# Kernel tuning notes

Hardware: AMD Instinct MI355X
Metric: run time of the kernel (lower is better)

## Reference

```python
import jax, jax.numpy as jnp
import numpy as np

NUM_HEADS = 16
HEAD_DIM = 64
HIDDEN = NUM_HEADS * HEAD_DIM
LN_EPS = 1e-6


def setup_inputs() -> dict:
    key = jax.random.key(0)
    ks = jax.random.split(key, 5)
    B, T, H = 2, 2048, HIDDEN
    s = 1.0 / np.sqrt(H)
    return {
        "h": jax.random.normal(ks[0], (B, T, H), jnp.float32),
        "Wq": jax.random.normal(ks[1], (H, H), jnp.float32) * s,
        "bq": jnp.zeros((H,), jnp.float32),
        "Wk": jax.random.normal(ks[2], (H, H), jnp.float32) * s,
        "bk": jnp.zeros((H,), jnp.float32),
        "Wv": jax.random.normal(ks[3], (H, H), jnp.float32) * s,
        "bv": jnp.zeros((H,), jnp.float32),
        "Wo": jax.random.normal(ks[4], (H, H), jnp.float32) * s,
        "bo": jnp.zeros((H,), jnp.float32),
        "gamma": jnp.ones((H,), jnp.float32),
        "beta": jnp.zeros((H,), jnp.float32),
    }


def _split_heads(x):
    B, T, H = x.shape
    return x.reshape(B, T, NUM_HEADS, HEAD_DIM).transpose(0, 2, 1, 3)  # [B,h,T,d]


def reference(h, Wq, bq, Wk, bk, Wv, bv, Wo, bo, gamma, beta):
    # QKV projections (nn.Linear: x @ W^T + b)
    Q = _split_heads(h @ Wq.T + bq)
    K = _split_heads(h @ Wk.T + bk)
    V = _split_heads(h @ Wv.T + bv)
    scale = HEAD_DIM ** -0.5
    scores = jnp.einsum("bhqd,bhkd->bhqk", Q, K) * scale  # [B,h,T,T]
    attn = jax.nn.softmax(scores, axis=-1)
    ctx = jnp.einsum("bhqk,bhkd->bhqd", attn, V)          # [B,h,T,d]
    B, _, T, _ = ctx.shape
    ctx = ctx.transpose(0, 2, 1, 3).reshape(B, T, HIDDEN)
    out = ctx @ Wo.T + bo + h  # dropout is identity at eval
    # LayerNorm(eps=1e-6)
    mu = out.mean(-1, keepdims=True)
    var = jnp.mean((out - mu) ** 2, -1, keepdims=True)
    return (out - mu) * jax.lax.rsqrt(var + LN_EPS) * gamma + beta
```

## Files before the change

### kernel.cpp

```cpp
#include <hip/hip_runtime.h>
#include <hip/hip_bf16.h>

#define NH   16
#define HD   64
#define HID  1024
#define TSEQ 2048
#define BATCH 2
#define KSCALE 0.18033688011112042f

typedef __attribute__((ext_vector_type(4))) float f32x4;
typedef __attribute__((ext_vector_type(8))) short s16x8;
typedef __attribute__((ext_vector_type(4))) short s16x4;
typedef __attribute__((ext_vector_type(8))) _Float16 f16x8;
typedef __attribute__((ext_vector_type(4))) _Float16 f16x4;
typedef __attribute__((ext_vector_type(2))) _Float16 f16x2;

__device__ __forceinline__ unsigned short f2bf(float f) {
  union { float f; unsigned int u; } v; v.f = f;
  unsigned int r = v.u + 0x7fffu + ((v.u >> 16) & 1u);
  return (unsigned short)(r >> 16);
}
__device__ __forceinline__ float bf2f(unsigned short b) {
  union { unsigned int u; float f; } v; v.u = ((unsigned int)b) << 16; return v.f;
}

__device__ __forceinline__ void gll16(const void* g, void* l) {
  __builtin_amdgcn_global_load_lds(
      (const __attribute__((address_space(1))) unsigned int*)g,
      (__attribute__((address_space(3))) unsigned int*)l, 16, 0, 0);
}

__global__ __launch_bounds__(256) void cast_all_k(
    const float* __restrict__ h,
    const float* __restrict__ w0, const float* __restrict__ w1,
    const float* __restrict__ w2, const float* __restrict__ w3,
    unsigned short* __restrict__ hb, unsigned short* __restrict__ wbase) {
  int i = blockIdx.x * 256 + threadIdx.x;
  const float* src; unsigned short* dst; int idx; float sc = 1.f;
  if (i < 1048576) { src = h; dst = hb; idx = i; }
  else {
    int idx4 = i - 1048576;
    int w = idx4 >> 18;
    idx = idx4 & 262143;
    src = (w == 0) ? w0 : (w == 1) ? w1 : (w == 2) ? w2 : w3;
    dst = wbase + (size_t)(idx4 - idx) * 4;
    if (w == 1) sc = KSCALE;
  }
  float4 v = ((const float4*)src)[idx];
  ushort4 o;
  o.x = f2bf(v.x * sc); o.y = f2bf(v.y * sc); o.z = f2bf(v.z * sc); o.w = f2bf(v.w * sc);
  ((ushort4*)dst)[idx] = o;
}

__global__ __launch_bounds__(256) void gemm_qkv(
    const unsigned short* __restrict__ hb,
    const unsigned short* __restrict__ wcat,
    const float* __restrict__ bq, const float* __restrict__ bk, const float* __restrict__ bv,
    unsigned short* __restrict__ qo, unsigned short* __restrict__ ko,
    unsigned short* __restrict__ vto) {
  __shared__ unsigned short Ash[2][128 * 32];
  __shared__ unsigned short Bsh[2][128 * 32];
  const int tid = threadIdx.x, lane = tid & 63, wave = tid >> 6;
  const int l15 = lane & 15, quad = lane >> 4;
  const int wr = wave >> 1, wc = wave & 1;
  const int bn = blockIdx.x * 128, bm = blockIdx.y * 128;
  const char* Ab = (const char*)(hb + (size_t)bm * HID);
  const char* Bb = (const char*)(wcat + (size_t)bn * HID);
  const int off = tid * 16;
  const int r0 = off >> 6, c0 = off & 63;
  const size_t ga0 = (size_t)r0 * (HID * 2) + c0;
  const size_t ga1 = (size_t)(r0 + 64) * (HID * 2) + c0;
  const int lb0 = wave * 512;
  const int lb1 = 2048 + wave * 512;

  f32x4 acc[4][4];
#pragma unroll
  for (int i = 0; i < 4; ++i)
#pragma unroll
    for (int j = 0; j < 4; ++j) acc[i][j] = f32x4{0.f, 0.f, 0.f, 0.f};

  gll16(Ab + ga0, &Ash[0][lb0]);
  gll16(Ab + ga1, &Ash[0][lb1]);
  gll16(Bb + ga0, &Bsh[0][lb0]);
  gll16(Bb + ga1, &Bsh[0][lb1]);
  __syncthreads();

  for (int k0 = 0; k0 < HID; k0 += 32) {
    const int cur = (k0 >> 5) & 1;
    if (k0 + 32 < HID) {
      const size_t kb = (size_t)(k0 + 32) * 2;
      gll16(Ab + ga0 + kb, &Ash[cur ^ 1][lb0]);
      gll16(Ab + ga1 + kb, &Ash[cur ^ 1][lb1]);
      gll16(Bb + ga0 + kb, &Bsh[cur ^ 1][lb0]);
      gll16(Bb + ga1 + kb, &Bsh[cur ^ 1][lb1]);
    }
    s16x8 af[4], bfr[4];
#pragma unroll
    for (int i = 0; i < 4; ++i)
      af[i] = *(const s16x8*)(&Ash[cur][(wr * 64 + i * 16 + l15) * 32 + quad * 8]);
#pragma unroll
    for (int j = 0; j < 4; ++j)
      bfr[j] = *(const s16x8*)(&Bsh[cur][(wc * 64 + j * 16 + l15) * 32 + quad * 8]);
#pragma unroll
    for (int i = 0; i < 4; ++i)
#pragma unroll
      for (int j = 0; j < 4; ++j)
        acc[i][j] = __builtin_amdgcn_mfma_f32_16x16x32_bf16(af[i], bfr[j], acc[i][j], 0, 0, 0);
    __syncthreads();
  }

  const int mat = bn >> 10;
  const int cb = (bn & 1023) + wc * 64;
  const int rbase = bm + wr * 64;
  if (mat == 2) {
#pragma unroll
    for (int j = 0; j < 4; ++j) {
      const int coln = cb + j * 16 + l15;
      const int head = coln >> 6, d = coln & 63;
      const float bb = bv[coln];
#pragma unroll
      for (int i = 0; i < 4; ++i) {
        const int row0 = rbase + i * 16 + quad * 4;
        const int bI = row0 >> 11, t0 = row0 & 2047;
        unsigned short o[4];
#pragma unroll
        for (int r = 0; r < 4; ++r) {
          _Float16 hv = (_Float16)(acc[i][j][r] + bb);
          o[r] = __builtin_bit_cast(unsigned short, hv);
        }
        *(s16x4*)(vto + ((size_t)((bI * NH + head) * HD + d)) * TSEQ + t0) = *(const s16x4*)o;
      }
    }
  } else {
    unsigned short* dst = (mat == 0) ? qo : ko;
#pragma unroll
    for (int j = 0; j < 4; ++j) {
      const int coln = cb + j * 16 + l15;
      const int head = coln >> 6, d = coln & 63;
      const float bb = (mat == 0) ? bq[coln] : bk[coln] * KSCALE;
#pragma unroll
      for (int i = 0; i < 4; ++i) {
#pragma unroll
        for (int r = 0; r < 4; ++r) {
          const int row = rbase + i * 16 + quad * 4 + r;
          const int bI = row >> 11, t = row & 2047;
          dst[(((size_t)(bI * NH + head) * TSEQ) + t) * HD + d] = f2bf(acc[i][j][r] + bb);
        }
      }
    }
  }
}

__global__ __launch_bounds__(256) void gemm_out(
    const unsigned short* __restrict__ ctx, const unsigned short* __restrict__ wo,
    const float* __restrict__ bo, const float* __restrict__ hres,
    float* __restrict__ outf) {
  __shared__ unsigned short Ash[2][128 * 32];
  __shared__ unsigned short Bsh[2][64 * 32];
  const int tid = threadIdx.x, lane = tid & 63, wave = tid >> 6;
  const int l15 = lane & 15, quad = lane >> 4;
  const int wr = wave >> 1, wc = wave & 1;
  const int bn = blockIdx.x * 64, bm = blockIdx.y * 128;
  const char* Ab = (const char*)(ctx + (size_t)bm * HID);
  const char* Bb = (const char*)(wo + (size_t)bn * HID);
  const int off = tid * 16;
  const int r0 = off >> 6, c0 = off & 63;
  const size_t ga0 = (size_t)r0 * (HID * 2) + c0;
  const size_t ga1 = (size_t)(r0 + 64) * (HID * 2) + c0;
  const int lb0 = wave * 512, lb1 = 2048 + wave * 512;

  f32x4 acc[4][2];
#pragma unroll
  for (int i = 0; i < 4; ++i)
#pragma unroll
    for (int j = 0; j < 2; ++j) acc[i][j] = f32x4{0.f, 0.f, 0.f, 0.f};

  gll16(Ab + ga0, &Ash[0][lb0]);
  gll16(Ab + ga1, &Ash[0][lb1]);
  gll16(Bb + ga0, &Bsh[0][lb0]);
  __syncthreads();

  for (int k0 = 0; k0 < HID; k0 += 32) {
    const int cur = (k0 >> 5) & 1;
    if (k0 + 32 < HID) {
      const size_t kb = (size_t)(k0 + 32) * 2;
      gll16(Ab + ga0 + kb, &Ash[cur ^ 1][lb0]);
      gll16(Ab + ga1 + kb, &Ash[cur ^ 1][lb1]);
      gll16(Bb + ga0 + kb, &Bsh[cur ^ 1][lb0]);
    }
    s16x8 af[4], bfr[2];
#pragma unroll
    for (int i = 0; i < 4; ++i)
      af[i] = *(const s16x8*)(&Ash[cur][(wr * 64 + i * 16 + l15) * 32 + quad * 8]);
#pragma unroll
    for (int j = 0; j < 2; ++j)
      bfr[j] = *(const s16x8*)(&Bsh[cur][(wc * 32 + j * 16 + l15) * 32 + quad * 8]);
#pragma unroll
    for (int i = 0; i < 4; ++i)
#pragma unroll
      for (int j = 0; j < 2; ++j)
        acc[i][j] = __builtin_amdgcn_mfma_f32_16x16x32_bf16(af[i], bfr[j], acc[i][j], 0, 0, 0);
    __syncthreads();
  }
#pragma unroll
  for (int j = 0; j < 2; ++j) {
    const int col = bn + wc * 32 + j * 16 + l15;
    const float bb = bo[col];
#pragma unroll
    for (int i = 0; i < 4; ++i) {
#pragma unroll
      for (int r = 0; r < 4; ++r) {
        const int row = bm + wr * 64 + i * 16 + quad * 4 + r;
        const size_t o = (size_t)row * HID + col;
        outf[o] = acc[i][j][r] + bb + hres[o];
      }
    }
  }
}

__global__ __launch_bounds__(256, 2) void attn_k(
    const unsigned short* __restrict__ qb, const unsigned short* __restrict__ kb,
    const unsigned short* __restrict__ vt, unsigned short* __restrict__ ctx,
    unsigned short* __restrict__ Opart, float* __restrict__ rsumP,
    int lsplit, int ntiles) {
  __shared__ unsigned short Ksh[64 * 72];
  __shared__ unsigned short Vsh[64 * 72];

  const int tid = threadIdx.x, lane = tid & 63, wave = tid >> 6;
  const int l15 = lane & 15, quad = lane >> 4;
  const int z = blockIdx.z;
  const int b = z >> lsplit;
  const int part = z & ((1 << lsplit) - 1);
  const int h = blockIdx.y, qt = blockIdx.x;
  const size_t ho = ((size_t)(b * NH + h)) * TSEQ * HD;
  const unsigned short* Qh = qb + ho;
  const unsigned short* Kh = kb + ho;
  const unsigned short* Vh = vt + ho;
  const int q0 = qt * 128 + wave * 32;
  const int kt0 = part * ntiles;

  s16x8 qf[2][2];
#pragma unroll
  for (int s = 0; s < 2; ++s)
#pragma unroll
    for (int ks = 0; ks < 2; ++ks)
      qf[s][ks] = *(const s16x8*)(Qh + (size_t)(q0 + s * 16 + l15) * HD + ks * 32 + quad * 8);

  f32x4 accO[4][2];
  float rsum[2];
#pragma unroll
  for (int n2 = 0; n2 < 4; ++n2)
#pragma unroll
    for (int s = 0; s < 2; ++s) accO[n2][s] = f32x4{0.f, 0.f, 0.f, 0.f};
  rsum[0] = rsum[1] = 0.f;

  const int sr = tid >> 3, sc = (tid & 7) * 8;
  s16x8 kreg[2], vreg[2];
#pragma unroll
  for (int hf = 0; hf < 2; ++hf) {
    kreg[hf] = *(const s16x8*)(Kh + (size_t)(kt0 * 64 + sr + hf * 32) * HD + sc);
    vreg[hf] = *(const s16x8*)(Vh + (size_t)(sr + hf * 32) * TSEQ + kt0 * 64 + sc);
  }

  for (int kt = 0; kt < ntiles; ++kt) {
    __syncthreads();
#pragma unroll
    for (int hf = 0; hf < 2; ++hf) {
      *(s16x8*)(Ksh + (sr + hf * 32) * 72 + sc) = kreg[hf];
      *(s16x8*)(Vsh + (sr + hf * 32) * 72 + sc) = vreg[hf];
    }
    __syncthreads();
    if (kt + 1 < ntiles) {
      const int k0n = (kt0 + kt + 1) * 64;
#pragma unroll
      for (int hf = 0; hf < 2; ++hf) {
        kreg[hf] = *(const s16x8*)(Kh + (size_t)(k0n + sr + hf * 32) * HD + sc);
        vreg[hf] = *(const s16x8*)(Vh + (size_t)(sr + hf * 32) * TSEQ + k0n + sc);
      }
    }

    f32x4 accS[2][4];
#pragma unroll
    for (int s = 0; s < 2; ++s)
#pragma unroll
      for (int n = 0; n < 4; ++n) accS[s][n] = f32x4{0.f, 0.f, 0.f, 0.f};
#pragma unroll
    for (int ks = 0; ks < 2; ++ks) {
#pragma unroll
      for (int n = 0; n < 4; ++n) {
        s16x8 kf = *(const s16x8*)(Ksh + (n * 16 + l15) * 72 + ks * 32 + quad * 8);
#pragma unroll
        for (int s = 0; s < 2; ++s)
          accS[s][n] = __builtin_amdgcn_mfma_f32_16x16x32_bf16(kf, qf[s][ks], accS[s][n], 0, 0, 0);
      }
    }

    f16x4 pB[2][4];
#pragma unroll
    for (int s = 0; s < 2; ++s)
#pragma unroll
      for (int n = 0; n < 4; ++n) {
        float e0 = __builtin_amdgcn_exp2f(accS[s][n][0]);
        float e1 = __builtin_amdgcn_exp2f(accS[s][n][1]);
        float e2 = __builtin_amdgcn_exp2f(accS[s][n][2]);
        float e3 = __builtin_amdgcn_exp2f(accS[s][n][3]);
        rsum[s] += (e0 + e1) + (e2 + e3);
        f16x2 lo = __builtin_bit_cast(f16x2, __builtin_amdgcn_cvt_pkrtz(e0, e1));
        f16x2 hi = __builtin_bit_cast(f16x2, __builtin_amdgcn_cvt_pkrtz(e2, e3));
        pB[s][n] = f16x4{lo[0], lo[1], hi[0], hi[1]};
      }

#pragma unroll
    for (int n = 0; n < 4; ++n) {
#pragma unroll
      for (int n2 = 0; n2 < 4; ++n2) {
        f16x4 vA = *(const f16x4*)(Vsh + (n2 * 16 + l15) * 72 + n * 16 + quad * 4);
#pragma unroll
        for (int s = 0; s < 2; ++s)
          accO[n2][s] = __builtin_amdgcn_mfma_f32_16x16x16f16(vA, pB[s][n], accO[n2][s], 0, 0, 0);
      }
    }
  }

#pragma unroll
  for (int s = 0; s < 2; ++s) {
    float t = rsum[s];
    t += __shfl_xor(t, 16, 64);
    t += __shfl_xor(t, 32, 64);
    rsum[s] = t;
  }

  if (lsplit) {
    const int slot = (part * BATCH + b) * NH + h;
    const size_t ob = (size_t)slot * TSEQ * HD;
#pragma unroll
    for (int s = 0; s < 2; ++s) {
      const int t = q0 + s * 16 + l15;
#pragma unroll
      for (int n2 = 0; n2 < 4; ++n2) {
        const int d0 = n2 * 16 + quad * 4;
        unsigned short o[4];
#pragma unroll
        for (int r = 0; r < 4; ++r) o[r] = f2bf(accO[n2][s][r]);
        *(s16x4*)(Opart + ob + (size_t)t * HD + d0) = *(const s16x4*)o;
      }
    }
    if (quad == 0) {
      const size_t rb = (size_t)slot * TSEQ;
#pragma unroll
      for (int s = 0; s < 2; ++s)
        rsumP[rb + q0 + s * 16 + l15] = rsum[s];
    }
  } else {
#pragma unroll
    for (int s = 0; s < 2; ++s) {
      const int t = q0 + s * 16 + l15;
      const float inv = 1.f / rsum[s];
#pragma unroll
      for (int n2 = 0; n2 < 4; ++n2) {
        const int d0 = n2 * 16 + quad * 4;
        unsigned short o[4];
#pragma unroll
        for (int r = 0; r < 4; ++r) o[r] = f2bf(accO[n2][s][r] * inv);
        *(s16x4*)(ctx + ((size_t)(b * TSEQ + t)) * HID + h * HD + d0) = *(const s16x4*)o;
      }
    }
  }
}

__global__ __launch_bounds__(256) void combine_k(
    const unsigned short* __restrict__ Opart, const float* __restrict__ rsumP,
    unsigned short* __restrict__ ctx, int nparts) {
  const int gtid = blockIdx.x * 256 + threadIdx.x;
  const int d = (gtid & 7) * 8;
  const int rem = gtid >> 3;
  const int t = rem & 2047;
  const int bh = rem >> 11;
  float acc[8] = {0, 0, 0, 0, 0, 0, 0, 0};
  float rs = 0.f;
  for (int p = 0; p < nparts; ++p) {
    const int slot = p * 32 + bh;
    s16x8 a = *(const s16x8*)(Opart + ((size_t)slot * TSEQ + t) * HD + d);
#pragma unroll
    for (int j = 0; j < 8; ++j) acc[j] += bf2f(((const unsigned short*)&a)[j]);
    rs += rsumP[(size_t)slot * TSEQ + t];
  }
  const float inv = 1.f / rs;
  unsigned short o[8];
#pragma unroll
  for (int j = 0; j < 8; ++j) o[j] = f2bf(acc[j] * inv);
  const int b = bh >> 4, h = bh & 15;
  *(s16x8*)(ctx + ((size_t)(b * TSEQ + t)) * HID + h * HD + d) = *(const s16x8*)o;
}

__global__ __launch_bounds__(256) void ln_k(float* __restrict__ io,
                                            const float* __restrict__ gamma,
                                            const float* __restrict__ beta) {
  const int row = blockIdx.x, tid = threadIdx.x;
  float x[4]; float s = 0.f, s2 = 0.f;
#pragma unroll
  for (int i = 0; i < 4; ++i) {
    x[i] = io[(size_t)row * HID + tid + i * 256];
    s += x[i]; s2 += x[i] * x[i];
  }
#pragma unroll
  for (int off = 1; off < 64; off <<= 1) {
    s  += __shfl_xor(s, off, 64);
    s2 += __shfl_xor(s2, off, 64);
  }
  __shared__ float red[8];
  const int wave = tid >> 6;
  if ((tid & 63) == 0) { red[wave] = s; red[wave + 4] = s2; }
  __syncthreads();
  s  = red[0] + red[1] + red[2] + red[3];
  s2 = red[4] + red[5] + red[6] + red[7];
  const float mean = s * (1.f / HID);
  const float var  = s2 * (1.f / HID) - mean * mean;
  const float rstd = rsqrtf(var + 1e-6f);
#pragma unroll
  for (int i = 0; i < 4; ++i) {
    const int col = tid + i * 256;
    io[(size_t)row * HID + col] = (x[i] - mean) * rstd * gamma[col] + beta[col];
  }
}

extern "C" void kernel_launch(void* const* d_in, const int* in_sizes, int n_in,
                              void* d_out, int out_size, void* d_ws, size_t ws_size,
                              hipStream_t stream) {
  const float* h    = (const float*)d_in[0];
  const float* Wq   = (const float*)d_in[1];
  const float* bq   = (const float*)d_in[2];
  const float* Wk   = (const float*)d_in[3];
  const float* bk   = (const float*)d_in[4];
  const float* Wv   = (const float*)d_in[5];
  const float* bv   = (const float*)d_in[6];
  const float* Wo   = (const float*)d_in[7];
  const float* bo   = (const float*)d_in[8];
  const float* gamma = (const float*)d_in[9];
  const float* beta  = (const float*)d_in[10];
  float* out = (float*)d_out;

  unsigned short* hb   = (unsigned short*)d_ws;
  unsigned short* wqb  = hb  + 4194304;
  unsigned short* wkb  = wqb + 1048576;
  unsigned short* wvb  = wkb + 1048576;
  unsigned short* wob  = wvb + 1048576;
  unsigned short* qb   = wob + 1048576;
  unsigned short* kb   = qb  + 4194304;
  unsigned short* vtf  = kb  + 4194304;
  unsigned short* Opart = vtf + 4194304;
  unsigned short* ctxb = hb;

  const size_t base = (size_t)(vtf + 4194304 - hb) * 2;
  int lsplit = 0;
  if (ws_size >= base + 2u * 8388608 + 2u * 262144) lsplit = 1;
  const int nparts = 1 << lsplit;
  float* rsumP = (float*)(Opart + (size_t)nparts * 4194304);

  cast_all_k<<<8192, 256, 0, stream>>>(h, Wq, Wk, Wv, Wo, hb, wqb);
  gemm_qkv<<<dim3(24, 32), 256, 0, stream>>>(hb, wqb, bq, bk, bv, qb, kb, vtf);
  attn_k<<<dim3(TSEQ / 128, NH, BATCH << lsplit), 256, 0, stream>>>(
      qb, kb, vtf, ctxb, Opart, rsumP, lsplit, 32 >> lsplit);
  if (lsplit)
    combine_k<<<2048, 256, 0, stream>>>(Opart, rsumP, ctxb, nparts);
  gemm_out<<<dim3(16, 32), 256, 0, stream>>>(ctxb, wob, bo, h, out);
  ln_k<<<4096, 256, 0, stream>>>(out, gamma, beta);
}
```

Measured before the change: 235.9 us.

## Triple-buffer GEMM LDS tiles with swizzled layout and one barrier per k-step

Both projection GEMMs move from double to triple buffering of LDS tiles. Each k-step now uses a single explicit vmcnt wait plus barrier, replacing the trailing __syncthreads, so global-to-LDS loads run two stages ahead of the MFMA work. The global source column is XOR-swizzled by row, and the LDS read offset is swizzled to match, to cut LDS bank conflicts on fragment reads. The cost is more LDS per block, which may lower occupancy, and reliance on hand-counted vmcnt values being correct.

```diff
diff --git a/kernel.cpp b/kernel.cpp
--- a/kernel.cpp
+++ b/kernel.cpp
@@ -29,6 +29,12 @@
       (const __attribute__((address_space(1))) unsigned int*)g,
       (__attribute__((address_space(3))) unsigned int*)l, 16, 0, 0);
 }
+
+#define WAITBAR(N)                                                      \
+  do {                                                                  \
+    __builtin_amdgcn_sched_barrier(0);                                  \
+    asm volatile("s_waitcnt vmcnt(" #N ")\n\ts_barrier" ::: "memory");  \
+  } while (0)
 
 __global__ __launch_bounds__(256) void cast_all_k(
     const float* __restrict__ h,
@@ -58,8 +64,8 @@
     const float* __restrict__ bq, const float* __restrict__ bk, const float* __restrict__ bv,
     unsigned short* __restrict__ qo, unsigned short* __restrict__ ko,
     unsigned short* __restrict__ vto) {
-  __shared__ unsigned short Ash[2][128 * 32];
-  __shared__ unsigned short Bsh[2][128 * 32];
+  __shared__ unsigned short Ash[3][128 * 32];
+  __shared__ unsigned short Bsh[3][128 * 32];
   const int tid = threadIdx.x, lane = tid & 63, wave = tid >> 6;
   const int l15 = lane & 15, quad = lane >> 4;
   const int wr = wave >> 1, wc = wave & 1;
@@ -67,9 +73,11 @@
   const char* Ab = (const char*)(hb + (size_t)bm * HID);
   const char* Bb = (const char*)(wcat + (size_t)bn * HID);
   const int off = tid * 16;
-  const int r0 = off >> 6, c0 = off & 63;
+  const int r0 = off >> 6;
+  const int q0i = (off >> 4) & 3;
+  const int c0 = (q0i ^ (r0 & 3)) << 4;
   const size_t ga0 = (size_t)r0 * (HID * 2) + c0;
-  const size_t ga1 = (size_t)(r0 + 64) * (HID * 2) + c0;
+  const size_t ga1 = ga0 + (size_t)64 * (HID * 2);
   const int lb0 = wave * 512;
   const int lb1 = 2048 + wave * 512;
 
@@ -79,35 +87,42 @@
 #pragma unroll
     for (int j = 0; j < 4; ++j) acc[i][j] = f32x4{0.f, 0.f, 0.f, 0.f};
 
-  gll16(Ab + ga0, &Ash[0][lb0]);
-  gll16(Ab + ga1, &Ash[0][lb1]);
-  gll16(Bb + ga0, &Bsh[0][lb0]);
-  gll16(Bb + ga1, &Bsh[0][lb1]);
-  __syncthreads();
-
-  for (int k0 = 0; k0 < HID; k0 += 32) {
-    const int cur = (k0 >> 5) & 1;
-    if (k0 + 32 < HID) {
-      const size_t kb = (size_t)(k0 + 32) * 2;
-      gll16(Ab + ga0 + kb, &Ash[cur ^ 1][lb0]);
-      gll16(Ab + ga1 + kb, &Ash[cur ^ 1][lb1]);
-      gll16(Bb + ga0 + kb, &Bsh[cur ^ 1][lb0]);
-      gll16(Bb + ga1 + kb, &Bsh[cur ^ 1][lb1]);
-    }
+  auto stage = [&](int bufi, int k0) {
+    const size_t kb = (size_t)k0 * 2;
+    gll16(Ab + ga0 + kb, &Ash[bufi][lb0]);
+    gll16(Ab + ga1 + kb, &Ash[bufi][lb1]);
+    gll16(Bb + ga0 + kb, &Bsh[bufi][lb0]);
+    gll16(Bb + ga1 + kb, &Bsh[bufi][lb1]);
+  };
+  const int qx = (quad ^ (l15 & 3)) * 8;
+  auto compute = [&](int bufi) {
     s16x8 af[4], bfr[4];
 #pragma unroll
     for (int i = 0; i < 4; ++i)
-      af[i] = *(const s16x8*)(&Ash[cur][(wr * 64 + i * 16 + l15) * 32 + quad * 8]);
+      af[i] = *(const s16x8*)(&Ash[bufi][(wr * 64 + i * 16 + l15) * 32 + qx]);
 #pragma unroll
     for (int j = 0; j < 4; ++j)
-      bfr[j] = *(const s16x8*)(&Bsh[cur][(wc * 64 + j * 16 + l15) * 32 + quad * 8]);
+      bfr[j] = *(const s16x8*)(&Bsh[bufi][(wc * 64 + j * 16 + l15) * 32 + qx]);
 #pragma unroll
     for (int i = 0; i < 4; ++i)
 #pragma unroll
       for (int j = 0; j < 4; ++j)
         acc[i][j] = __builtin_amdgcn_mfma_f32_16x16x32_bf16(af[i], bfr[j], acc[i][j], 0, 0, 0);
-    __syncthreads();
-  }
+  };
+
+  stage(0, 0);
+  stage(1, 32);
+  int cur = 0, pf = 2;
+  const int NT = HID / 32;
+  for (int t = 0; t < NT - 1; ++t) {
+    WAITBAR(4);
+    if (t + 2 < NT) stage(pf, (t + 2) * 32);
+    compute(cur);
+    cur = (cur == 2) ? 0 : cur + 1;
+    pf  = (pf  == 2) ? 0 : pf + 1;
+  }
+  WAITBAR(0);
+  compute(cur);
 
   const int mat = bn >> 10;
   const int cb = (bn & 1023) + wc * 64;
@@ -155,8 +170,8 @@
     const unsigned short* __restrict__ ctx, const unsigned short* __restrict__ wo,
     const float* __restrict__ bo, const float* __restrict__ hres,
     float* __restrict__ outf) {
-  __shared__ unsigned short Ash[2][128 * 32];
-  __shared__ unsigned short Bsh[2][64 * 32];
+  __shared__ unsigned short Ash[3][128 * 32];
+  __shared__ unsigned short Bsh[3][64 * 32];
   const int tid = threadIdx.x, lane = tid & 63, wave = tid >> 6;
   const int l15 = lane & 15, quad = lane >> 4;
   const int wr = wave >> 1, wc = wave & 1;
@@ -164,9 +179,11 @@
   const char* Ab = (const char*)(ctx + (size_t)bm * HID);
   const char* Bb = (const char*)(wo + (size_t)bn * HID);
   const int off = tid * 16;
-  const int r0 = off >> 6, c0 = off & 63;
+  const int r0 = off >> 6;
+  const int q0i = (off >> 4) & 3;
+  const int c0 = (q0i ^ (r0 & 3)) << 4;
   const size_t ga0 = (size_t)r0 * (HID * 2) + c0;
-  const size_t ga1 = (size_t)(r0 + 64) * (HID * 2) + c0;
+  const size_t ga1 = ga0 + (size_t)64 * (HID * 2);
   const int lb0 = wave * 512, lb1 = 2048 + wave * 512;
 
   f32x4 acc[4][2];
@@ -175,33 +192,42 @@
 #pragma unroll
     for (int j = 0; j < 2; ++j) acc[i][j] = f32x4{0.f, 0.f, 0.f, 0.f};
 
-  gll16(Ab + ga0, &Ash[0][lb0]);
-  gll16(Ab + ga1, &Ash[0][lb1]);
-  gll16(Bb + ga0, &Bsh[0][lb0]);
-  __syncthreads();
-
-  for (int k0 = 0; k0 < HID; k0 += 32) {
-    const int cur = (k0 >> 5) & 1;
-    if (k0 + 32 < HID) {
-      const size_t kb = (size_t)(k0 + 32) * 2;
-      gll16(Ab + ga0 + kb, &Ash[cur ^ 1][lb0]);
-      gll16(Ab + ga1 + kb, &Ash[cur ^ 1][lb1]);
-      gll16(Bb + ga0 + kb, &Bsh[cur ^ 1][lb0]);
-    }
+  auto stage = [&](int bufi, int k0) {
+    const size_t kb = (size_t)k0 * 2;
+    gll16(Ab + ga0 + kb, &Ash[bufi][lb0]);
+    gll16(Ab + ga1 + kb, &Ash[bufi][lb1]);
+    gll16(Bb + ga0 + kb, &Bsh[bufi][lb0]);
+  };
+  const int qx = (quad ^ (l15 & 3)) * 8;
+  auto compute = [&](int bufi) {
     s16x8 af[4], bfr[2];
 #pragma unroll
     for (int i = 0; i < 4; ++i)
-      af[i] = *(const s16x8*)(&Ash[cur][(wr * 64 + i * 16 + l15) * 32 + quad * 8]);
+      af[i] = *(const s16x8*)(&Ash[bufi][(wr * 64 + i * 16 + l15) * 32 + qx]);
 #pragma unroll
     for (int j = 0; j < 2; ++j)
-      bfr[j] = *(const s16x8*)(&Bsh[cur][(wc * 32 + j * 16 + l15) * 32 + quad * 8]);
+      bfr[j] = *(const s16x8*)(&Bsh[bufi][(wc * 32 + j * 16 + l15) * 32 + qx]);
 #pragma unroll
     for (int i = 0; i < 4; ++i)
 #pragma unroll
       for (int j = 0; j < 2; ++j)
         acc[i][j] = __builtin_amdgcn_mfma_f32_16x16x32_bf16(af[i], bfr[j], acc[i][j], 0, 0, 0);
-    __syncthreads();
-  }
+  };
+
+  stage(0, 0);
+  stage(1, 32);
+  int cur = 0, pf = 2;
+  const int NT = HID / 32;
+  for (int t = 0; t < NT - 1; ++t) {
+    WAITBAR(3);
+    if (t + 2 < NT) stage(pf, (t + 2) * 32);
+    compute(cur);
+    cur = (cur == 2) ? 0 : cur + 1;
+    pf  = (pf  == 2) ? 0 : pf + 1;
+  }
+  WAITBAR(0);
+  compute(cur);
+
 #pragma unroll
   for (int j = 0; j < 2; ++j) {
     const int col = bn + wc * 32 + j * 16 + l15;
```

Result: no change. 234.9 us (-0.5%).
